# Performance work log

Hardware: AMD Instinct MI355X
Metric: run time of the kernel (lower is better)

The kernel has to match this reference:

```python
import jax, jax.numpy as jnp
import numpy as np

MARGIN = 0.1  # init kwarg


def setup_inputs() -> dict:
    key = jax.random.key(0)
    k1, k2, k3 = jax.random.split(key, 3)
    B, P, D = 256, 64, 1024
    imFtr = jax.random.normal(k1, (B, P, D), dtype=jnp.float32)
    disFtr = jax.random.normal(k2, (B, D), dtype=jnp.float32)
    lblList = jax.random.randint(k3, (B,), 0, 100000, dtype=jnp.int64 if jax.config.read('jax_enable_x64') else jnp.int32)
    return {"imFtr": imFtr, "disFtr": disFtr, "lblList": lblList}


def reference(imFtr, disFtr, lblList):
    B, P, D = imFtr.shape
    # simMM: [B*P, B] -> [B, P, B]; max over proposals P -> simMax [B, B]
    simMM = jnp.einsum('bpd,cd->bpc', imFtr, disFtr)
    simMax = jnp.max(simMM, axis=1)  # [B, B] (rows: image/video i, cols: text j)
    pos = jnp.diagonal(simMax)       # [B]

    # valid negative pairs: labels differ (diagonal excluded automatically)
    mask = (lblList[:, None] != lblList[None, :]).astype(simMax.dtype)  # [B, B]
    pairNum = jnp.sum(mask)

    # image -> text ranking: relu(sim[i, j] - sim[i, i] + margin)
    loss_it = jnp.sum(jnp.maximum(simMax - pos[:, None] + MARGIN, 0.0) * mask)
    loss = loss_it / pairNum

    # biLossFlag: text -> image ranking: relu(sim[j, i] - sim[i, i] + margin)
    loss_ti = jnp.sum(jnp.maximum(simMax - pos[None, :] + MARGIN, 0.0) * mask)
    loss = loss + jnp.where(pairNum > 0, loss_ti / pairNum, 0.0)

    return loss.reshape(1)
```

## Files before the change

### kernel.cpp

```cpp
#include <hip/hip_runtime.h>

constexpr int NB = 256;
constexpr int NP = 64;
constexpr int ND = 1024;
constexpr float MARGIN = 0.1f;

typedef __attribute__((ext_vector_type(8))) short bf16x8;
typedef __attribute__((ext_vector_type(4))) short bf16x4;
typedef __attribute__((ext_vector_type(4))) float f32x4;

static __device__ inline unsigned short f2bf(float f) {
  unsigned u = __builtin_bit_cast(unsigned, f);
  u += 0x7fffu + ((u >> 16) & 1u);
  return (unsigned short)(u >> 16);
}

static __device__ inline bf16x4 cvt4(float4 a) {
  bf16x4 r;
  r[0] = (short)f2bf(a.x); r[1] = (short)f2bf(a.y);
  r[2] = (short)f2bf(a.z); r[3] = (short)f2bf(a.w);
  return r;
}

__global__ __launch_bounds__(256) void cvtB_kernel(
    const float* __restrict__ src, short* __restrict__ dst,
    unsigned* __restrict__ ticket) {
  if (blockIdx.x == 0 && threadIdx.x == 0) atomicExch(ticket, 0u);
  const int idx = (blockIdx.x * 256 + threadIdx.x) * 4;
  float4 v = *reinterpret_cast<const float4*>(src + idx);
  *reinterpret_cast<bf16x4*>(dst + idx) = cvt4(v);
}

__global__ __launch_bounds__(1024, 4) void simmax_kernel(
    const float* __restrict__ imFtr, const short* __restrict__ disB,
    float* __restrict__ simMax) {
  const int i  = blockIdx.x;
  const int t  = threadIdx.x;
  const int w  = t >> 6;
  const int l  = t & 63;
  const int lr = l & 15;
  const int lk = l >> 4;

  __shared__ short Asl[2][NP][256];

  f32x4 acc[4];
#pragma unroll
  for (int pt = 0; pt < 4; ++pt)
#pragma unroll
    for (int r = 0; r < 4; ++r) acc[pt][r] = 0.0f;

  const int ar = t >> 4;
  const int aj = t & 15;
  const float* abase = imFtr + ((size_t)i * NP + ar) * ND + aj * 4;
  float4 areg[4];

  const short* bp = disB + (size_t)(w * 16 + lr) * ND + lk * 8;
  bf16x8 breg[8];

#define STAGE_LOAD(C)                                                        \
  _Pragma("unroll")                                                          \
  for (int g = 0; g < 4; ++g)                                                \
    areg[g] = *reinterpret_cast<const float4*>(abase + (C) * 256 + g * 64);

#define STAGE_WRITE(BUF)                                                     \
  _Pragma("unroll")                                                          \
  for (int g = 0; g < 4; ++g) {                                              \
    const int s  = g * 8 + (aj >> 1);                                        \
    const int so = (s ^ (ar & 15)) * 8 + (aj & 1) * 4;                       \
    *reinterpret_cast<bf16x4*>(&Asl[BUF][ar][so]) = cvt4(areg[g]);           \
  }

  STAGE_LOAD(0);
#pragma unroll
  for (int j = 0; j < 8; ++j)
    breg[j] = *reinterpret_cast<const bf16x8*>(bp + j * 32);
  STAGE_WRITE(0);
  __syncthreads();

#pragma unroll
  for (int c = 0; c < 4; ++c) {
    const int cb = c & 1;
    if (c < 3) STAGE_LOAD(c + 1);
#pragma unroll
    for (int j8 = 0; j8 < 8; ++j8) {
      const int jj = c * 8 + j8;
      const int so = ((j8 * 4 + lk) ^ lr) * 8;
      bf16x8 a0 = *reinterpret_cast<const bf16x8*>(&Asl[cb][lr][so]);
      bf16x8 a1 = *reinterpret_cast<const bf16x8*>(&Asl[cb][16 + lr][so]);
      bf16x8 a2 = *reinterpret_cast<const bf16x8*>(&Asl[cb][32 + lr][so]);
      bf16x8 a3 = *reinterpret_cast<const bf16x8*>(&Asl[cb][48 + lr][so]);
      acc[0] = __builtin_amdgcn_mfma_f32_16x16x32_bf16(a0, breg[j8], acc[0], 0, 0, 0);
      acc[1] = __builtin_amdgcn_mfma_f32_16x16x32_bf16(a1, breg[j8], acc[1], 0, 0, 0);
      acc[2] = __builtin_amdgcn_mfma_f32_16x16x32_bf16(a2, breg[j8], acc[2], 0, 0, 0);
      acc[3] = __builtin_amdgcn_mfma_f32_16x16x32_bf16(a3, breg[j8], acc[3], 0, 0, 0);
      if (jj + 8 < 32)
        breg[j8] = *reinterpret_cast<const bf16x8*>(bp + (jj + 8) * 32);
    }
    if (c < 3) {
      STAGE_WRITE(cb ^ 1);
      __syncthreads();
    }
  }

#undef STAGE_LOAD
#undef STAGE_WRITE

  float m = acc[0][0];
#pragma unroll
  for (int pt = 0; pt < 4; ++pt)
#pragma unroll
    for (int r = 0; r < 4; ++r) m = fmaxf(m, acc[pt][r]);
  m = fmaxf(m, __shfl_xor(m, 16));
  m = fmaxf(m, __shfl_xor(m, 32));
  if (l < 16) simMax[(size_t)i * NB + w * 16 + lr] = m;
}

__global__ __launch_bounds__(256) void loss_tail_kernel(
    const float* __restrict__ simMax, const int* __restrict__ lbl,
    float* __restrict__ partial, float* __restrict__ out,
    unsigned* __restrict__ ticket) {
  const int i = blockIdx.x;
  const int j = threadIdx.x;
  __shared__ float posi_sh;
  __shared__ float red[3][4];
  __shared__ int winner_sh;

  float s = simMax[(size_t)i * NB + j];
  if (j == i) posi_sh = s;
  __syncthreads();
  const float posi = posi_sh;
  const float posj = simMax[(size_t)j * NB + j];

  const float msk = (lbl[i] != lbl[j]) ? 1.0f : 0.0f;
  float c  = msk;
  float l1 = msk * fmaxf(s - posi + MARGIN, 0.0f);
  float l2 = msk * fmaxf(s - posj + MARGIN, 0.0f);
#pragma unroll
  for (int o = 32; o > 0; o >>= 1) {
    c  += __shfl_down(c, o);
    l1 += __shfl_down(l1, o);
    l2 += __shfl_down(l2, o);
  }
  const int w = j >> 6;
  if ((j & 63) == 0) { red[0][w] = c; red[1][w] = l1; red[2][w] = l2; }
  __syncthreads();
  if (j == 0) {
    __hip_atomic_store(&partial[i * 3 + 0],
                       red[0][0] + red[0][1] + red[0][2] + red[0][3],
                       __ATOMIC_RELAXED, __HIP_MEMORY_SCOPE_AGENT);
    __hip_atomic_store(&partial[i * 3 + 1],
                       red[1][0] + red[1][1] + red[1][2] + red[1][3],
                       __ATOMIC_RELAXED, __HIP_MEMORY_SCOPE_AGENT);
    __hip_atomic_store(&partial[i * 3 + 2],
                       red[2][0] + red[2][1] + red[2][2] + red[2][3],
                       __ATOMIC_RELAXED, __HIP_MEMORY_SCOPE_AGENT);
  }
  __syncthreads();
  if (j == 0) {
    unsigned old = __hip_atomic_fetch_add(ticket, 1u, __ATOMIC_RELAXED,
                                          __HIP_MEMORY_SCOPE_AGENT);
    winner_sh = (old == 255u) ? 1 : 0;
  }
  __syncthreads();
  if (!winner_sh) return;
  if (j == 0)
    (void)__hip_atomic_load(ticket, __ATOMIC_ACQUIRE, __HIP_MEMORY_SCOPE_AGENT);
  __syncthreads();

  float fc  = partial[j * 3 + 0];
  float fl1 = partial[j * 3 + 1];
  float fl2 = partial[j * 3 + 2];
#pragma unroll
  for (int o = 32; o > 0; o >>= 1) {
    fc  += __shfl_down(fc, o);
    fl1 += __shfl_down(fl1, o);
    fl2 += __shfl_down(fl2, o);
  }
  if ((j & 63) == 0) { red[0][w] = fc; red[1][w] = fl1; red[2][w] = fl2; }
  __syncthreads();
  if (j == 0) {
    float cs  = red[0][0] + red[0][1] + red[0][2] + red[0][3];
    float l1s = red[1][0] + red[1][1] + red[1][2] + red[1][3];
    float l2s = red[2][0] + red[2][1] + red[2][2] + red[2][3];
    float loss = l1s / cs;
    loss += (cs > 0.0f) ? (l2s / cs) : 0.0f;
    out[0] = loss;
  }
}

extern "C" void kernel_launch(void* const* d_in, const int* in_sizes, int n_in,
                              void* d_out, int out_size, void* d_ws, size_t ws_size,
                              hipStream_t stream) {
  (void)in_sizes; (void)n_in; (void)out_size; (void)ws_size;
  const float* imFtr  = (const float*)d_in[0];
  const float* disFtr = (const float*)d_in[1];
  const int*   lbl    = (const int*)d_in[2];
  float* out = (float*)d_out;

  const size_t disB_bytes = (size_t)NB * ND * sizeof(short);
  const size_t sim_bytes  = (size_t)NB * NB * sizeof(float);
  const size_t par_bytes  = (size_t)NB * 3 * sizeof(float);

  short*    disB    = (short*)d_ws;
  float*    simMax  = (float*)((char*)d_ws + disB_bytes);
  float*    partial = (float*)((char*)d_ws + disB_bytes + sim_bytes);
  unsigned* ticket  = (unsigned*)((char*)d_ws + disB_bytes + sim_bytes + par_bytes);

  cvtB_kernel<<<dim3(NB), dim3(256), 0, stream>>>(disFtr, disB, ticket);
  simmax_kernel<<<dim3(NB), dim3(1024), 0, stream>>>(imFtr, disB, simMax);
  loss_tail_kernel<<<dim3(NB), dim3(256), 0, stream>>>(simMax, lbl, partial, out, ticket);
}
```

Before: 36.58 us.

## Switch GEMM to 32x32x16 MFMA tiles and split tail into separate finalize kernel

The similarity GEMM now has each wave compute a 32x32 tile with the 32x32x16 bf16 MFMA instead of four 16x16x32 tiles. The 16 waves are split into two proposal halves whose per-column maxima are merged through shared memory with an extra block barrier. This halves the LDS A-fragment reads per MFMA and uses fewer, larger matrix instructions. The atomic ticket last-block reduction is also replaced by a separate single-block finalize kernel, which removes the atomics but adds one more launch.

Result: slower. 48.48 us (+32.5%).

```diff
diff --git a/kernel.cpp b/kernel.cpp
--- a/kernel.cpp
+++ b/kernel.cpp
@@ -7,7 +7,7 @@
 
 typedef __attribute__((ext_vector_type(8))) short bf16x8;
 typedef __attribute__((ext_vector_type(4))) short bf16x4;
-typedef __attribute__((ext_vector_type(4))) float f32x4;
+typedef __attribute__((ext_vector_type(16))) float f32x16;
 
 static __device__ inline unsigned short f2bf(float f) {
   unsigned u = __builtin_bit_cast(unsigned, f);
@@ -23,9 +23,7 @@
 }
 
 __global__ __launch_bounds__(256) void cvtB_kernel(
-    const float* __restrict__ src, short* __restrict__ dst,
-    unsigned* __restrict__ ticket) {
-  if (blockIdx.x == 0 && threadIdx.x == 0) atomicExch(ticket, 0u);
+    const float* __restrict__ src, short* __restrict__ dst) {
   const int idx = (blockIdx.x * 256 + threadIdx.x) * 4;
   float4 v = *reinterpret_cast<const float4*>(src + idx);
   *reinterpret_cast<bf16x4*>(dst + idx) = cvt4(v);
@@ -38,24 +36,22 @@
   const int t  = threadIdx.x;
   const int w  = t >> 6;
   const int l  = t & 63;
-  const int lr = l & 15;
-  const int lk = l >> 4;
+  const int lc = l & 31;
+  const int hi = l >> 5;
+  const int ph = w >> 3;
+  const int cg = w & 7;
 
   __shared__ short Asl[2][NP][256];
+  __shared__ float Red[8][32];
 
-  f32x4 acc[4];
+  f32x16 acc;
 #pragma unroll
-  for (int pt = 0; pt < 4; ++pt)
-#pragma unroll
-    for (int r = 0; r < 4; ++r) acc[pt][r] = 0.0f;
+  for (int r = 0; r < 16; ++r) acc[r] = 0.0f;
 
   const int ar = t >> 4;
   const int aj = t & 15;
   const float* abase = imFtr + ((size_t)i * NP + ar) * ND + aj * 4;
   float4 areg[4];
-
-  const short* bp = disB + (size_t)(w * 16 + lr) * ND + lk * 8;
-  bf16x8 breg[8];
 
 #define STAGE_LOAD(C)                                                        \
   _Pragma("unroll")                                                          \
@@ -70,10 +66,16 @@
     *reinterpret_cast<bf16x4*>(&Asl[BUF][ar][so]) = cvt4(areg[g]);           \
   }
 
+  const short* bp = disB + (size_t)(cg * 32 + lc) * ND + hi * 8;
+  bf16x8 breg[8];
+
+  const int row = ph * 32 + lc;
+  const int r15 = row & 15;
+
   STAGE_LOAD(0);
 #pragma unroll
   for (int j = 0; j < 8; ++j)
-    breg[j] = *reinterpret_cast<const bf16x8*>(bp + j * 32);
+    breg[j] = *reinterpret_cast<const bf16x8*>(bp + j * 16);
   STAGE_WRITE(0);
   __syncthreads();
 
@@ -82,19 +84,13 @@
     const int cb = c & 1;
     if (c < 3) STAGE_LOAD(c + 1);
 #pragma unroll
-    for (int j8 = 0; j8 < 8; ++j8) {
-      const int jj = c * 8 + j8;
-      const int so = ((j8 * 4 + lk) ^ lr) * 8;
-      bf16x8 a0 = *reinterpret_cast<const bf16x8*>(&Asl[cb][lr][so]);
-      bf16x8 a1 = *reinterpret_cast<const bf16x8*>(&Asl[cb][16 + lr][so]);
-      bf16x8 a2 = *reinterpret_cast<const bf16x8*>(&Asl[cb][32 + lr][so]);
-      bf16x8 a3 = *reinterpret_cast<const bf16x8*>(&Asl[cb][48 + lr][so]);
-      acc[0] = __builtin_amdgcn_mfma_f32_16x16x32_bf16(a0, breg[j8], acc[0], 0, 0, 0);
-      acc[1] = __builtin_amdgcn_mfma_f32_16x16x32_bf16(a1, breg[j8], acc[1], 0, 0, 0);
-      acc[2] = __builtin_amdgcn_mfma_f32_16x16x32_bf16(a2, breg[j8], acc[2], 0, 0, 0);
-      acc[3] = __builtin_amdgcn_mfma_f32_16x16x32_bf16(a3, breg[j8], acc[3], 0, 0, 0);
-      if (jj + 8 < 32)
-        breg[j8] = *reinterpret_cast<const bf16x8*>(bp + (jj + 8) * 32);
+    for (int j8 = 0; j8 < 16; ++j8) {
+      const int jj = c * 16 + j8;
+      const int so = ((j8 * 2 + hi) ^ r15) * 8;
+      bf16x8 a = *reinterpret_cast<const bf16x8*>(&Asl[cb][row][so]);
+      acc = __builtin_amdgcn_mfma_f32_32x32x16_bf16(a, breg[jj & 7], acc, 0, 0, 0);
+      if (jj + 8 < 64)
+        breg[jj & 7] = *reinterpret_cast<const bf16x8*>(bp + (jj + 8) * 16);
     }
     if (c < 3) {
       STAGE_WRITE(cb ^ 1);
@@ -105,25 +101,24 @@
 #undef STAGE_LOAD
 #undef STAGE_WRITE
 
-  float m = acc[0][0];
+  float m = acc[0];
 #pragma unroll
-  for (int pt = 0; pt < 4; ++pt)
-#pragma unroll
-    for (int r = 0; r < 4; ++r) m = fmaxf(m, acc[pt][r]);
-  m = fmaxf(m, __shfl_xor(m, 16));
+  for (int r = 1; r < 16; ++r) m = fmaxf(m, acc[r]);
   m = fmaxf(m, __shfl_xor(m, 32));
-  if (l < 16) simMax[(size_t)i * NB + w * 16 + lr] = m;
+
+  if (ph == 0 && l < 32) Red[cg][lc] = m;
+  __syncthreads();
+  if (ph == 1 && l < 32)
+    simMax[(size_t)i * NB + cg * 32 + lc] = fmaxf(m, Red[cg][lc]);
 }
 
-__global__ __launch_bounds__(256) void loss_tail_kernel(
+__global__ __launch_bounds__(256) void loss_kernel(
     const float* __restrict__ simMax, const int* __restrict__ lbl,
-    float* __restrict__ partial, float* __restrict__ out,
-    unsigned* __restrict__ ticket) {
+    float* __restrict__ partial) {
   const int i = blockIdx.x;
   const int j = threadIdx.x;
   __shared__ float posi_sh;
   __shared__ float red[3][4];
-  __shared__ int winner_sh;
 
   float s = simMax[(size_t)i * NB + j];
   if (j == i) posi_sh = s;
@@ -145,40 +140,29 @@
   if ((j & 63) == 0) { red[0][w] = c; red[1][w] = l1; red[2][w] = l2; }
   __syncthreads();
   if (j == 0) {
-    __hip_atomic_store(&partial[i * 3 + 0],
-                       red[0][0] + red[0][1] + red[0][2] + red[0][3],
-                       __ATOMIC_RELAXED, __HIP_MEMORY_SCOPE_AGENT);
-    __hip_atomic_store(&partial[i * 3 + 1],
-                       red[1][0] + red[1][1] + red[1][2] + red[1][3],
-                       __ATOMIC_RELAXED, __HIP_MEMORY_SCOPE_AGENT);
-    __hip_atomic_store(&partial[i * 3 + 2],
-                       red[2][0] + red[2][1] + red[2][2] + red[2][3],
-                       __ATOMIC_RELAXED, __HIP_MEMORY_SCOPE_AGENT);
+    partial[i * 3 + 0] = red[0][0] + red[0][1] + red[0][2] + red[0][3];
+    partial[i * 3 + 1] = red[1][0] + red[1][1] + red[1][2] + red[1][3];
+    partial[i * 3 + 2] = red[2][0] + red[2][1] + red[2][2] + red[2][3];
   }
-  __syncthreads();
-  if (j == 0) {
-    unsigned old = __hip_atomic_fetch_add(ticket, 1u, __ATOMIC_RELAXED,
-                                          __HIP_MEMORY_SCOPE_AGENT);
-    winner_sh = (old == 255u) ? 1 : 0;
-  }
-  __syncthreads();
-  if (!winner_sh) return;
-  if (j == 0)
-    (void)__hip_atomic_load(ticket, __ATOMIC_ACQUIRE, __HIP_MEMORY_SCOPE_AGENT);
-  __syncthreads();
+}
 
-  float fc  = partial[j * 3 + 0];
-  float fl1 = partial[j * 3 + 1];
-  float fl2 = partial[j * 3 + 2];
+__global__ __launch_bounds__(256) void finalize_kernel(
+    const float* __restrict__ partial, float* __restrict__ out) {
+  const int t = threadIdx.x;
+  __shared__ float red[3][4];
+  float c  = partial[t * 3 + 0];
+  float l1 = partial[t * 3 + 1];
+  float l2 = partial[t * 3 + 2];
 #pragma unroll
   for (int o = 32; o > 0; o >>= 1) {
-    fc  += __shfl_down(fc, o);
-    fl1 += __shfl_down(fl1, o);
-    fl2 += __shfl_down(fl2, o);
+    c  += __shfl_down(c, o);
+    l1 += __shfl_down(l1, o);
+    l2 += __shfl_down(l2, o);
   }
-  if ((j & 63) == 0) { red[0][w] = fc; red[1][w] = fl1; red[2][w] = fl2; }
+  const int w = t >> 6;
+  if ((t & 63) == 0) { red[0][w] = c; red[1][w] = l1; red[2][w] = l2; }
   __syncthreads();
-  if (j == 0) {
+  if (t == 0) {
     float cs  = red[0][0] + red[0][1] + red[0][2] + red[0][3];
     float l1s = red[1][0] + red[1][1] + red[1][2] + red[1][3];
     float l2s = red[2][0] + red[2][1] + red[2][2] + red[2][3];
@@ -199,14 +183,13 @@
 
   const size_t disB_bytes = (size_t)NB * ND * sizeof(short);
   const size_t sim_bytes  = (size_t)NB * NB * sizeof(float);
-  const size_t par_bytes  = (size_t)NB * 3 * sizeof(float);
 
-  short*    disB    = (short*)d_ws;
-  float*    simMax  = (float*)((char*)d_ws + disB_bytes);
-  float*    partial = (float*)((char*)d_ws + disB_bytes + sim_bytes);
-  unsigned* ticket  = (unsigned*)((char*)d_ws + disB_bytes + sim_bytes + par_bytes);
+  short* disB    = (short*)d_ws;
+  float* simMax  = (float*)((char*)d_ws + disB_bytes);
+  float* partial = (float*)((char*)d_ws + disB_bytes + sim_bytes);
 
-  cvtB_kernel<<<dim3(NB), dim3(256), 0, stream>>>(disFtr, disB, ticket);
+  cvtB_kernel<<<dim3(NB), dim3(256), 0, stream>>>(disFtr, disB);
   simmax_kernel<<<dim3(NB), dim3(1024), 0, stream>>>(imFtr, disB, simMax);
-  loss_tail_kernel<<<dim3(NB), dim3(256), 0, stream>>>(simMax, lbl, partial, out, ticket);
+  loss_kernel<<<dim3(NB), dim3(256), 0, stream>>>(simMax, lbl, partial);
+  finalize_kernel<<<dim3(1), dim3(256), 0, stream>>>(partial, out);
 }
```
